# Optimization experiments

Measured on AMD Instinct MI355X. Metric: run time of the kernel, lower is better.

Reference implementation:

```python
import jax, jax.numpy as jnp
import numpy as np

N = 384        # n_res
C = 128        # c_pair
H = 4          # num_head
DH = C // H    # qkv_dim = 32
LN_EPS = 1e-5
NEG_INF = -1e9


def setup_inputs() -> dict:
    key = jax.random.key(0)
    ks = jax.random.split(key, 8)
    s = 0.02
    return {
        "pair": jax.random.normal(ks[0], (N, N, C), dtype=jnp.float32),
        "mask": jax.random.randint(ks[1], (N, N), 0, 2, dtype=jnp.int32),
        "ln_w": jnp.ones((C,), dtype=jnp.float32),
        "ln_b": jnp.zeros((C,), dtype=jnp.float32),
        "w_bias": jax.random.normal(ks[2], (C, H), dtype=jnp.float32) * s,
        "wq": jax.random.normal(ks[3], (C, C), dtype=jnp.float32) * s,
        "wk": jax.random.normal(ks[4], (C, C), dtype=jnp.float32) * s,
        "wv": jax.random.normal(ks[5], (C, C), dtype=jnp.float32) * s,
        "wg": jax.random.normal(ks[6], (C, C), dtype=jnp.float32) * s,
        "wo": jax.random.normal(ks[7], (C, C), dtype=jnp.float32) * s,
    }


def reference(pair, mask, ln_w, ln_b, w_bias, wq, wk, wv, wg, wo):
    # LayerNorm over c_pair (biased variance, as torch)
    mu = pair.mean(-1, keepdims=True)
    var = jnp.mean(jnp.square(pair - mu), axis=-1, keepdims=True)
    x = (pair - mu) * jax.lax.rsqrt(var + LN_EPS) * ln_w + ln_b  # [N,N,C]

    # per-head pair bias: [H, N, N] (query axis q, key axis k)
    bias = jnp.einsum('qkc,ch->hqk', x, w_bias)

    # QKV + gating projections (no bias)
    q = jnp.einsum('bkc,cd->bkd', x, wq).reshape(N, N, H, DH)
    k = jnp.einsum('bkc,cd->bkd', x, wk).reshape(N, N, H, DH)
    v = jnp.einsum('bkc,cd->bkd', x, wv).reshape(N, N, H, DH)

    scale = 1.0 / np.sqrt(DH).astype(np.float32)
    logits = jnp.einsum('bqhd,bkhd->bhqk', q, k) * scale + bias[None]  # [N,H,N,N]
    # mask[b, k]: disallow attending to masked keys in row b
    logits = jnp.where(mask[:, None, None, :] > 0, logits, NEG_INF)
    probs = jax.nn.softmax(logits, axis=-1)

    o = jnp.einsum('bhqk,bkhd->bqhd', probs, v).reshape(N, N, C)
    gate = jax.nn.sigmoid(jnp.einsum('bqc,cd->bqd', x, wg))
    out = jnp.einsum('bqc,cd->bqd', o * gate, wo)  # [N,N,C]
    return out
```

## Files before the change

### kernel.cpp

```cpp
#include <hip/hip_runtime.h>
#include <hip/hip_bf16.h>
#include <stdint.h>

#define NRES 384
#define CPAIR 128
#define NHEAD 4
#define DHEAD 32
#define MROWS (NRES * NRES)
#define QK_SCALE 0.17677669529663687f
#define LOG2E 1.4426950408889634f
#define QK_L2E (0.17677669529663687f * 1.4426950408889634f)

typedef unsigned short u16;
typedef short bf16x8 __attribute__((ext_vector_type(8)));
typedef float f32x4 __attribute__((ext_vector_type(4)));

__device__ __forceinline__ u16 f2bf(float f) {
  union { float f; uint32_t u; } c; c.f = f;
  uint32_t u = c.u + 0x7fff + ((c.u >> 16) & 1);
  return (u16)(u >> 16);
}
__device__ __forceinline__ float bf2f(u16 h) {
  union { uint32_t u; float f; } c; c.u = ((uint32_t)h) << 16; return c.f;
}
__device__ __forceinline__ float fast_exp2(float x) {
#if __has_builtin(__builtin_amdgcn_exp2f)
  return __builtin_amdgcn_exp2f(x);
#else
  return exp2f(x);
#endif
}
__device__ __forceinline__ uint32_t cvt_pk_bf16(float lo, float hi) {
  uint32_t r;
  asm("v_cvt_pk_bf16_f32 %0, %1, %2" : "=v"(r) : "v"(lo), "v"(hi));
  return r;
}

__global__ void prep_kernel(const float* __restrict__ wq, const float* __restrict__ wk,
                            const float* __restrict__ wv, const float* __restrict__ wg,
                            const float* __restrict__ wb, const float* __restrict__ wo,
                            u16* __restrict__ wcat, u16* __restrict__ wot) {
  int tid = blockIdx.x * blockDim.x + threadIdx.x;
  int stride = gridDim.x * blockDim.x;
  for (int i = tid; i < 576 * 128; i += stride) {
    int n = i >> 7, kk = i & 127;
    float val;
    if (n < 128)      val = wq[kk * 128 + n] * QK_L2E;
    else if (n < 256) val = wk[kk * 128 + (n - 128)];
    else if (n < 384) val = wv[kk * 128 + (n - 256)];
    else if (n < 512) val = wg[kk * 128 + (n - 384)];
    else if (n < 516) val = wb[kk * 4 + (n - 512)] * LOG2E;
    else              val = 0.f;
    wcat[i] = f2bf(val);
  }
  for (int i = tid; i < 128 * 128; i += stride) {
    int n = i >> 7, kk = i & 127;
    wot[i] = f2bf(wo[kk * 128 + n]);
  }
}

__global__ __launch_bounds__(256) void proj_kernel(
    const float* __restrict__ pair, const float* __restrict__ lnw,
    const float* __restrict__ lnb, const u16* __restrict__ wcat,
    u16* __restrict__ q, u16* __restrict__ k, u16* __restrict__ v,
    u16* __restrict__ g, float* __restrict__ biasL) {
  __shared__ __align__(16) u16 xs[64 * 136];
  __shared__ __align__(16) u16 wsm[64 * 136];
  const int m0 = blockIdx.x * 64;
  const int tid = threadIdx.x;
  {
    const int row = tid >> 2, q4 = tid & 3;
    const float* pr = pair + (size_t)(m0 + row) * CPAIR + q4 * 32;
    float4 vals[8];
    float s1 = 0.f, s2 = 0.f;
#pragma unroll
    for (int i = 0; i < 8; ++i) {
      vals[i] = ((const float4*)pr)[i];
      s1 += (vals[i].x + vals[i].y) + (vals[i].z + vals[i].w);
      s2 += vals[i].x * vals[i].x + vals[i].y * vals[i].y +
            vals[i].z * vals[i].z + vals[i].w * vals[i].w;
    }
    s1 += __shfl_xor(s1, 1); s1 += __shfl_xor(s1, 2);
    s2 += __shfl_xor(s2, 1); s2 += __shfl_xor(s2, 2);
    const float mu = s1 * (1.f / 128.f);
    const float rs = rsqrtf(s2 * (1.f / 128.f) - mu * mu + 1e-5f);
    const float* wr = lnw + q4 * 32;
    const float* br = lnb + q4 * 32;
    uint32_t packed[16];
#pragma unroll
    for (int i = 0; i < 8; ++i) {
      float4 w4 = ((const float4*)wr)[i];
      float4 b4 = ((const float4*)br)[i];
      float y0 = (vals[i].x - mu) * rs * w4.x + b4.x;
      float y1 = (vals[i].y - mu) * rs * w4.y + b4.y;
      float y2 = (vals[i].z - mu) * rs * w4.z + b4.z;
      float y3 = (vals[i].w - mu) * rs * w4.w + b4.w;
      packed[i * 2]     = (uint32_t)f2bf(y0) | ((uint32_t)f2bf(y1) << 16);
      packed[i * 2 + 1] = (uint32_t)f2bf(y2) | ((uint32_t)f2bf(y3) << 16);
    }
#pragma unroll
    for (int i = 0; i < 4; ++i)
      *(uint4*)&xs[row * 136 + q4 * 32 + i * 8] = *(uint4*)&packed[i * 4];
  }
  const int w = tid >> 6, lane = tid & 63, lm = lane & 15, quad = lane >> 4;
  for (int nc = 0; nc < 9; ++nc) {
    __syncthreads();
#pragma unroll
    for (int i = 0; i < 4; ++i) {
      int c = tid + i * 256;
      int row = c >> 4, col8 = (c & 15) * 8;
      *(uint4*)&wsm[row * 136 + col8] =
          *(const uint4*)&wcat[(size_t)(nc * 64 + row) * CPAIR + col8];
    }
    __syncthreads();
    f32x4 acc[4] = {{0, 0, 0, 0}, {0, 0, 0, 0}, {0, 0, 0, 0}, {0, 0, 0, 0}};
#pragma unroll
    for (int ks = 0; ks < 4; ++ks) {
      bf16x8 a = *(const bf16x8*)&xs[(w * 16 + lm) * 136 + ks * 32 + quad * 8];
#pragma unroll
      for (int nt = 0; nt < 4; ++nt) {
        bf16x8 bb = *(const bf16x8*)&wsm[(nt * 16 + lm) * 136 + ks * 32 + quad * 8];
        acc[nt] = __builtin_amdgcn_mfma_f32_16x16x32_bf16(a, bb, acc[nt], 0, 0, 0);
      }
    }
#pragma unroll
    for (int nt = 0; nt < 4; ++nt) {
      int n = nc * 64 + nt * 16 + lm;
#pragma unroll
      for (int r = 0; r < 4; ++r) {
        size_t m = (size_t)(m0 + w * 16 + quad * 4 + r);
        float val = acc[nt][r];
        if (n < 128)      q[m * CPAIR + n] = f2bf(val);
        else if (n < 256) k[m * CPAIR + (n - 128)] = f2bf(val);
        else if (n < 384) v[m * CPAIR + (n - 256)] = f2bf(val);
        else if (n < 512) g[m * CPAIR + (n - 384)] = f2bf(1.f / (1.f + __expf(-val)));
        else if (n < 516) {
          int h = n - 512;
          int q_idx = (int)(m / NRES), k_idx = (int)(m % NRES);
          int qt = q_idx >> 6, l6 = q_idx & 63;
          int ww = l6 >> 4, lmq = l6 & 15;
          int t = k_idx >> 4, qk = (k_idx >> 2) & 3, rk = k_idx & 3;
          size_t idx = ((size_t)((h * 6 + qt) * 24 + t) * 256 +
                        (ww * 64 + qk * 16 + lmq)) * 4 + rk;
          biasL[idx] = val;
        }
      }
    }
  }
}

__global__ __launch_bounds__(512, 4) void attn_kernel(
    const u16* __restrict__ q, const u16* __restrict__ k, const u16* __restrict__ v,
    const u16* __restrict__ g, const float* __restrict__ biasL, const int* __restrict__ mask,
    u16* __restrict__ og) {
  __shared__ __align__(16) u16 Ks[NRES * 40];
  __shared__ __align__(16) u16 Vt[DHEAD * 392];
  __shared__ __align__(16) float mskb[NRES];

  const int b = blockIdx.x, h = blockIdx.y;
  const int tid = threadIdx.x;
  const int w = tid >> 6, lane = tid & 63, lm = lane & 15, quad = lane >> 4;
  const int wv = w & 3, hi = w >> 2;

  const u16* kb = k + (size_t)(b * NRES) * CPAIR + h * DHEAD;
  const u16* vb = v + (size_t)(b * NRES) * CPAIR + h * DHEAD;
  for (int i = tid; i < NRES * 4; i += 512) {
    int kk = i >> 2, c8 = (i & 3) * 8;
    *(uint4*)&Ks[kk * 40 + c8] = *(const uint4*)&kb[(size_t)kk * CPAIR + c8];
  }
  for (int i = tid; i < NRES * 4; i += 512) {
    int d8 = i & 3, kk = i >> 2;
    bf16x8 val = *(const bf16x8*)&vb[(size_t)kk * CPAIR + d8 * 8];
    int G = (kk >> 5) * 4 + ((kk >> 2) & 3);
    int e = (kk & 3) + 4 * ((kk >> 4) & 1);
    int col = (((G ^ d8) << 3) | e);
#pragma unroll
    for (int j = 0; j < 8; ++j) Vt[(d8 * 8 + j) * 392 + col] = (u16)val[j];
  }
  for (int i = tid; i < NRES; i += 512)
    mskb[i] = (mask[b * NRES + i] > 0) ? 0.f : -4096.f;
  __syncthreads();

  const int f0 = lm >> 3, f1 = (lm + 16) >> 3;

  for (int it = 0; it < 3; ++it) {
    const int qt = hi * 3 + it;
    const int q0 = qt * 64;
    bf16x8 af = *(const bf16x8*)&q[(size_t)(b * NRES + q0 + wv * 16 + lm) * CPAIR +
                                   h * DHEAD + quad * 8];
    const float* bptr = biasL + ((size_t)(h * 6 + qt) * 24) * 1024 + (wv * 64 + lane) * 4;

    float gv0[4], gv1[4];
#pragma unroll
    for (int r = 0; r < 4; ++r) {
      size_t mrow = (size_t)(b * NRES + q0 + wv * 16 + quad * 4 + r);
      gv0[r] = bf2f(g[mrow * CPAIR + h * DHEAD + lm]);
      gv1[r] = bf2f(g[mrow * CPAIR + h * DHEAD + 16 + lm]);
    }

    f32x4 bvp[2][2];
    bvp[0][0] = *(const f32x4*)(bptr + 0 * 1024);
    bvp[0][1] = *(const f32x4*)(bptr + 1 * 1024);
    bvp[1][0] = *(const f32x4*)(bptr + 2 * 1024);
    bvp[1][1] = *(const f32x4*)(bptr + 3 * 1024);

    float rsum = 0.f;
    f32x4 o0 = {0, 0, 0, 0}, o1 = {0, 0, 0, 0};
#pragma unroll
    for (int c = 0; c < 12; ++c) {
      const int t0 = c * 2, t1 = c * 2 + 1;
      f32x4 mq0 = *(const f32x4*)&mskb[t0 * 16 + quad * 4];
      f32x4 mq1 = *(const f32x4*)&mskb[t1 * 16 + quad * 4];
      f32x4 cv0 = bvp[c & 1][0] + mq0;
      f32x4 cv1 = bvp[c & 1][1] + mq1;
      if (c < 10) {
        bvp[c & 1][0] = *(const f32x4*)(bptr + (t0 + 4) * 1024);
        bvp[c & 1][1] = *(const f32x4*)(bptr + (t1 + 4) * 1024);
      }
      bf16x8 kf0 = *(const bf16x8*)&Ks[(t0 * 16 + lm) * 40 + quad * 8];
      bf16x8 kf1 = *(const bf16x8*)&Ks[(t1 * 16 + lm) * 40 + quad * 8];
      __builtin_amdgcn_s_setprio(1);
      f32x4 s0 = __builtin_amdgcn_mfma_f32_16x16x32_bf16(kf0, af, cv0, 0, 0, 0);
      f32x4 s1 = __builtin_amdgcn_mfma_f32_16x16x32_bf16(kf1, af, cv1, 0, 0, 0);
      __builtin_amdgcn_s_setprio(0);
      float p00 = fast_exp2(s0[0]), p01 = fast_exp2(s0[1]);
      float p02 = fast_exp2(s0[2]), p03 = fast_exp2(s0[3]);
      float p10 = fast_exp2(s1[0]), p11 = fast_exp2(s1[1]);
      float p12 = fast_exp2(s1[2]), p13 = fast_exp2(s1[3]);
      rsum += ((p00 + p01) + (p02 + p03)) + ((p10 + p11) + (p12 + p13));
      union { uint32_t u[4]; bf16x8 v8; } pf;
      pf.u[0] = cvt_pk_bf16(p00, p01);
      pf.u[1] = cvt_pk_bf16(p02, p03);
      pf.u[2] = cvt_pk_bf16(p10, p11);
      pf.u[3] = cvt_pk_bf16(p12, p13);
      int B0i = c * 4 + quad;
      bf16x8 vt0 = *(const bf16x8*)&Vt[lm * 392 + ((B0i ^ f0) << 3)];
      bf16x8 vt1 = *(const bf16x8*)&Vt[(lm + 16) * 392 + ((B0i ^ f1) << 3)];
      __builtin_amdgcn_s_setprio(1);
      o0 = __builtin_amdgcn_mfma_f32_16x16x32_bf16(pf.v8, vt0, o0, 0, 0, 0);
      o1 = __builtin_amdgcn_mfma_f32_16x16x32_bf16(pf.v8, vt1, o1, 0, 0, 0);
      __builtin_amdgcn_s_setprio(0);
    }
    rsum += __shfl_xor(rsum, 16);
    rsum += __shfl_xor(rsum, 32);
#pragma unroll
    for (int r = 0; r < 4; ++r) {
      float rall = __shfl(rsum, quad * 4 + r);
      float rinv = 1.f / rall;
      size_t mrow = (size_t)(b * NRES + q0 + wv * 16 + quad * 4 + r);
      int c0 = h * DHEAD + lm, c1 = h * DHEAD + 16 + lm;
      og[mrow * CPAIR + c0] = f2bf(o0[r] * rinv * gv0[r]);
      og[mrow * CPAIR + c1] = f2bf(o1[r] * rinv * gv1[r]);
    }
  }
}

__global__ __launch_bounds__(256) void outproj_kernel(const u16* __restrict__ og,
                                                      const u16* __restrict__ wot,
                                                      float* __restrict__ out) {
  __shared__ __align__(16) u16 xs[64 * 136];
  __shared__ __align__(16) u16 wsm[64 * 136];
  const int m0 = blockIdx.x * 64;
  const int tid = threadIdx.x;
#pragma unroll
  for (int i = 0; i < 4; ++i) {
    int c = tid + i * 256;
    int row = c >> 4, col8 = (c & 15) * 8;
    *(uint4*)&xs[row * 136 + col8] = *(const uint4*)&og[(size_t)(m0 + row) * CPAIR + col8];
  }
  const int w = tid >> 6, lane = tid & 63, lm = lane & 15, quad = lane >> 4;
  for (int nc = 0; nc < 2; ++nc) {
    __syncthreads();
#pragma unroll
    for (int i = 0; i < 4; ++i) {
      int c = tid + i * 256;
      int row = c >> 4, col8 = (c & 15) * 8;
      *(uint4*)&wsm[row * 136 + col8] =
          *(const uint4*)&wot[(size_t)(nc * 64 + row) * CPAIR + col8];
    }
    __syncthreads();
    f32x4 acc[4] = {{0, 0, 0, 0}, {0, 0, 0, 0}, {0, 0, 0, 0}, {0, 0, 0, 0}};
#pragma unroll
    for (int ks = 0; ks < 4; ++ks) {
      bf16x8 a = *(const bf16x8*)&xs[(w * 16 + lm) * 136 + ks * 32 + quad * 8];
#pragma unroll
      for (int nt = 0; nt < 4; ++nt) {
        bf16x8 bb = *(const bf16x8*)&wsm[(nt * 16 + lm) * 136 + ks * 32 + quad * 8];
        acc[nt] = __builtin_amdgcn_mfma_f32_16x16x32_bf16(a, bb, acc[nt], 0, 0, 0);
      }
    }
#pragma unroll
    for (int nt = 0; nt < 4; ++nt) {
      int n = nc * 64 + nt * 16 + lm;
#pragma unroll
      for (int r = 0; r < 4; ++r) {
        size_t m = (size_t)(m0 + w * 16 + quad * 4 + r);
        out[m * CPAIR + n] = acc[nt][r];
      }
    }
  }
}

extern "C" void kernel_launch(void* const* d_in, const int* in_sizes, int n_in,
                              void* d_out, int out_size, void* d_ws, size_t ws_size,
                              hipStream_t stream) {
  const float* pair = (const float*)d_in[0];
  const int* mask = (const int*)d_in[1];
  const float* ln_w = (const float*)d_in[2];
  const float* ln_b = (const float*)d_in[3];
  const float* w_bias = (const float*)d_in[4];
  const float* wq = (const float*)d_in[5];
  const float* wk = (const float*)d_in[6];
  const float* wv = (const float*)d_in[7];
  const float* wg = (const float*)d_in[8];
  const float* wo = (const float*)d_in[9];
  float* out = (float*)d_out;

  u16* qb = (u16*)d_out;
  u16* gb = qb + (size_t)MROWS * CPAIR;

  char* ws = (char*)d_ws;
  const size_t SZ = (size_t)MROWS * CPAIR * 2;
  u16* og = (u16*)(ws);
  u16* kb = (u16*)(ws + SZ);
  u16* vb = (u16*)(ws + 2 * SZ);
  float* biasL = (float*)(ws + 3 * SZ);
  u16* wcat = (u16*)(ws + 3 * SZ + (size_t)NHEAD * MROWS * 4);
  u16* wot = wcat + 576 * 128;

  hipLaunchKernelGGL(prep_kernel, dim3(64), dim3(256), 0, stream,
                     wq, wk, wv, wg, w_bias, wo, wcat, wot);
  hipLaunchKernelGGL(proj_kernel, dim3(MROWS / 64), dim3(256), 0, stream,
                     pair, ln_w, ln_b, wcat, qb, kb, vb, gb, biasL);
  hipLaunchKernelGGL(attn_kernel, dim3(NRES, NHEAD), dim3(512), 0, stream,
                     qb, kb, vb, gb, biasL, mask, og);
  hipLaunchKernelGGL(outproj_kernel, dim3(MROWS / 64), dim3(256), 0, stream,
                     og, wot, out);
}
```

Before: 285.1 us.

## Software-pipeline QK logits one step ahead and trim padded projection chunk

The attention inner loop now computes the next step's QK^T MFMA before doing the exp/softmax and PV MFMA of the current step. This lets matrix-core work overlap with exp and bf16 conversion instead of stalling on the dependency. Separately, the last weight chunk of the fused projection kernel only holds the 4 bias columns, so the extra weight-tile loads and MFMAs for that chunk are skipped. The pipelining raises register pressure by keeping extra accumulators live.

```diff
diff --git a/kernel.cpp b/kernel.cpp
--- a/kernel.cpp
+++ b/kernel.cpp
@@ -107,6 +107,7 @@
     __syncthreads();
 #pragma unroll
     for (int i = 0; i < 4; ++i) {
+      if (nc == 8 && i > 0) break;
       int c = tid + i * 256;
       int row = c >> 4, col8 = (c & 15) * 8;
       *(uint4*)&wsm[row * 136 + col8] =
@@ -119,12 +120,14 @@
       bf16x8 a = *(const bf16x8*)&xs[(w * 16 + lm) * 136 + ks * 32 + quad * 8];
 #pragma unroll
       for (int nt = 0; nt < 4; ++nt) {
+        if (nc == 8 && nt > 0) continue;
         bf16x8 bb = *(const bf16x8*)&wsm[(nt * 16 + lm) * 136 + ks * 32 + quad * 8];
         acc[nt] = __builtin_amdgcn_mfma_f32_16x16x32_bf16(a, bb, acc[nt], 0, 0, 0);
       }
     }
 #pragma unroll
     for (int nt = 0; nt < 4; ++nt) {
+      if (nc == 8 && nt > 0) continue;
       int n = nc * 64 + nt * 16 + lm;
 #pragma unroll
       for (int r = 0; r < 4; ++r) {
@@ -204,29 +207,44 @@
     bvp[1][0] = *(const f32x4*)(bptr + 2 * 1024);
     bvp[1][1] = *(const f32x4*)(bptr + 3 * 1024);
 
+    f32x4 s_cur0, s_cur1;
+    {
+      f32x4 cv0 = bvp[0][0] + *(const f32x4*)&mskb[0 * 16 + quad * 4];
+      f32x4 cv1 = bvp[0][1] + *(const f32x4*)&mskb[1 * 16 + quad * 4];
+      bf16x8 kf0 = *(const bf16x8*)&Ks[(0 * 16 + lm) * 40 + quad * 8];
+      bf16x8 kf1 = *(const bf16x8*)&Ks[(1 * 16 + lm) * 40 + quad * 8];
+      __builtin_amdgcn_s_setprio(1);
+      s_cur0 = __builtin_amdgcn_mfma_f32_16x16x32_bf16(kf0, af, cv0, 0, 0, 0);
+      s_cur1 = __builtin_amdgcn_mfma_f32_16x16x32_bf16(kf1, af, cv1, 0, 0, 0);
+      __builtin_amdgcn_s_setprio(0);
+      bvp[0][0] = *(const f32x4*)(bptr + 4 * 1024);
+      bvp[0][1] = *(const f32x4*)(bptr + 5 * 1024);
+    }
+
     float rsum = 0.f;
     f32x4 o0 = {0, 0, 0, 0}, o1 = {0, 0, 0, 0};
 #pragma unroll
     for (int c = 0; c < 12; ++c) {
-      const int t0 = c * 2, t1 = c * 2 + 1;
-      f32x4 mq0 = *(const f32x4*)&mskb[t0 * 16 + quad * 4];
-      f32x4 mq1 = *(const f32x4*)&mskb[t1 * 16 + quad * 4];
-      f32x4 cv0 = bvp[c & 1][0] + mq0;
-      f32x4 cv1 = bvp[c & 1][1] + mq1;
-      if (c < 10) {
-        bvp[c & 1][0] = *(const f32x4*)(bptr + (t0 + 4) * 1024);
-        bvp[c & 1][1] = *(const f32x4*)(bptr + (t1 + 4) * 1024);
-      }
-      bf16x8 kf0 = *(const bf16x8*)&Ks[(t0 * 16 + lm) * 40 + quad * 8];
-      bf16x8 kf1 = *(const bf16x8*)&Ks[(t1 * 16 + lm) * 40 + quad * 8];
-      __builtin_amdgcn_s_setprio(1);
-      f32x4 s0 = __builtin_amdgcn_mfma_f32_16x16x32_bf16(kf0, af, cv0, 0, 0, 0);
-      f32x4 s1 = __builtin_amdgcn_mfma_f32_16x16x32_bf16(kf1, af, cv1, 0, 0, 0);
-      __builtin_amdgcn_s_setprio(0);
-      float p00 = fast_exp2(s0[0]), p01 = fast_exp2(s0[1]);
-      float p02 = fast_exp2(s0[2]), p03 = fast_exp2(s0[3]);
-      float p10 = fast_exp2(s1[0]), p11 = fast_exp2(s1[1]);
-      float p12 = fast_exp2(s1[2]), p13 = fast_exp2(s1[3]);
+      f32x4 s_n0 = {0, 0, 0, 0}, s_n1 = {0, 0, 0, 0};
+      if (c < 11) {
+        const int tn0 = (c + 1) * 2, tn1 = tn0 + 1;
+        f32x4 cv0 = bvp[(c + 1) & 1][0] + *(const f32x4*)&mskb[tn0 * 16 + quad * 4];
+        f32x4 cv1 = bvp[(c + 1) & 1][1] + *(const f32x4*)&mskb[tn1 * 16 + quad * 4];
+        bf16x8 kf0 = *(const bf16x8*)&Ks[(tn0 * 16 + lm) * 40 + quad * 8];
+        bf16x8 kf1 = *(const bf16x8*)&Ks[(tn1 * 16 + lm) * 40 + quad * 8];
+        __builtin_amdgcn_s_setprio(1);
+        s_n0 = __builtin_amdgcn_mfma_f32_16x16x32_bf16(kf0, af, cv0, 0, 0, 0);
+        s_n1 = __builtin_amdgcn_mfma_f32_16x16x32_bf16(kf1, af, cv1, 0, 0, 0);
+        __builtin_amdgcn_s_setprio(0);
+        if (c < 9) {
+          bvp[(c + 1) & 1][0] = *(const f32x4*)(bptr + ((c + 3) * 2) * 1024);
+          bvp[(c + 1) & 1][1] = *(const f32x4*)(bptr + ((c + 3) * 2 + 1) * 1024);
+        }
+      }
+      float p00 = fast_exp2(s_cur0[0]), p01 = fast_exp2(s_cur0[1]);
+      float p02 = fast_exp2(s_cur0[2]), p03 = fast_exp2(s_cur0[3]);
+      float p10 = fast_exp2(s_cur1[0]), p11 = fast_exp2(s_cur1[1]);
+      float p12 = fast_exp2(s_cur1[2]), p13 = fast_exp2(s_cur1[3]);
       rsum += ((p00 + p01) + (p02 + p03)) + ((p10 + p11) + (p12 + p13));
       union { uint32_t u[4]; bf16x8 v8; } pf;
       pf.u[0] = cvt_pk_bf16(p00, p01);
@@ -240,6 +258,8 @@
       o0 = __builtin_amdgcn_mfma_f32_16x16x32_bf16(pf.v8, vt0, o0, 0, 0, 0);
       o1 = __builtin_amdgcn_mfma_f32_16x16x32_bf16(pf.v8, vt1, o1, 0, 0, 0);
       __builtin_amdgcn_s_setprio(0);
+      s_cur0 = s_n0;
+      s_cur1 = s_n1;
     }
     rsum += __shfl_xor(rsum, 16);
     rsum += __shfl_xor(rsum, 32);
```

Result: slower. 331.6 us (+16.3%).
